# Optimization experiments

Measured on AMD Instinct MI355X. Metric: run time of the kernel, lower is better.

## Reference

```python
import jax, jax.numpy as jnp
import numpy as np

NUM_OBJ_CLS = 9  # len(anchor_scales) * len(anchor_ratios) = 3 * 3


def _bce_with_logits_sum(x, y):
    # Numerically stable BCEWithLogitsLoss(reduction='sum'):
    # max(x,0) - x*y + log(1 + exp(-|x|)), summed over all elements.
    return jnp.sum(jnp.maximum(x, 0.0) - x * y + jnp.log1p(jnp.exp(-jnp.abs(x))))


def setup_inputs() -> dict:
    key = jax.random.key(0)
    k1, k2, k3 = jax.random.split(key, 3)
    B, H, W = 16, 192, 192
    pred = jax.random.normal(k1, (B, 6 * NUM_OBJ_CLS, H, W), dtype=jnp.float32)
    target = jax.random.uniform(k2, (B, 6, H, W), dtype=jnp.float32)
    loc = jax.random.randint(k3, (128, 2), 0, H)  # (x, y) coords into HxW map
    return {"pred": pred, "target": target, "loc": loc}


def reference(pred, target, loc):
    # Objectness loss: for i in range(0, 18, 2):
    #   BCE_sum(pred[:, i], target[:, 0]) + BCE_sum(pred[:, i+1], target[:, 1])
    # then divided by NUM_OBJ_CLS. Even channels pair with target ch 0,
    # odd channels with target ch 1. Vectorized over the 9 anchor classes.
    even = pred[:, 0:2 * NUM_OBJ_CLS:2]   # [B, 9, H, W]
    odd = pred[:, 1:2 * NUM_OBJ_CLS:2]    # [B, 9, H, W]
    t0 = target[:, 0:1]                    # [B, 1, H, W] broadcasts over 9
    t1 = target[:, 1:2]
    loss_obj = (_bce_with_logits_sum(even, t0) + _bce_with_logits_sum(odd, t1))
    loss_obj = loss_obj / NUM_OBJ_CLS
    # NOTE: in the original module the box-loss branch computes pred_box /
    # target_box gathers inside python loops but never accumulates them into
    # loss_box, which stays 0. Faithfully, the output is loss_obj alone; loc
    # does not affect the result.
    return loss_obj
```

## Files before the change

kernel.cpp:

```cpp
#include <hip/hip_runtime.h>
#include <hip/hip_bf16.h>


#define HW_     (192 * 192)
#define HW4_    (HW_ / 4)
#define NCH_    18
#define PREDC_  54
#define TGTC_   6
#define NB_     16

__device__ __forceinline__ float bce_elem(float x, float y) {
    return fmaxf(x, 0.0f) - x * y + log1pf(__expf(-fabsf(x)));
}

__global__ __launch_bounds__(256) void rpn_bce_kernel(
        const float* __restrict__ pred,
        const float* __restrict__ target,
        float* __restrict__ out) {
    const int total = NB_ * NCH_ * HW4_;
    const int stride = gridDim.x * blockDim.x;

    const float4* __restrict__ p4 = (const float4*)pred;
    const float4* __restrict__ t4 = (const float4*)target;

    float acc = 0.0f;
    for (int i = blockIdx.x * blockDim.x + threadIdx.x; i < total; i += stride) {
        int b  = i / (NCH_ * HW4_);
        int r  = i - b * (NCH_ * HW4_);
        int c  = r / HW4_;
        int hw = r - c * HW4_;

        float4 x = p4[(b * PREDC_ + c) * HW4_ + hw];
        float4 y = t4[(b * TGTC_ + (c & 1)) * HW4_ + hw];

        acc += bce_elem(x.x, y.x);
        acc += bce_elem(x.y, y.y);
        acc += bce_elem(x.z, y.z);
        acc += bce_elem(x.w, y.w);
    }

    #pragma unroll
    for (int off = 32; off > 0; off >>= 1)
        acc += __shfl_down(acc, off, 64);

    __shared__ float wsum[4];
    const int lane = threadIdx.x & 63;
    const int wid  = threadIdx.x >> 6;
    if (lane == 0) wsum[wid] = acc;
    __syncthreads();

    if (threadIdx.x == 0) {
        float s = wsum[0] + wsum[1] + wsum[2] + wsum[3];
        atomicAdd(out, s * (1.0f / 9.0f));
    }
}

extern "C" void kernel_launch(void* const* d_in, const int* in_sizes, int n_in,
                              void* d_out, int out_size, void* d_ws, size_t ws_size,
                              hipStream_t stream) {
    const float* pred   = (const float*)d_in[0];
    const float* target = (const float*)d_in[1];
    float* out = (float*)d_out;

    hipMemsetAsync(out, 0, sizeof(float), stream);

    rpn_bce_kernel<<<2048, 256, 0, stream>>>(pred, target, out);
}
```

Before: 188.6 us.

## Reuse target load across nine anchor channels and drop grid-stride loop

Each thread now owns one (parity, batch, position) float4 of the target. It loads that target value once and loops, unrolled, over the nine anchor channels of matching parity. This replaces the grid-stride loop and its per-iteration integer divisions, removes redundant target reads, and exposes nine independent loads per thread. The launch grows to one thread per target vector (1152 blocks), with one atomic per block. log1pf is also swapped for the cheaper __logf(1+t), which is slightly less accurate.

```diff
diff --git a/kernel.cpp b/kernel.cpp
--- a/kernel.cpp
+++ b/kernel.cpp
@@ -1,38 +1,41 @@
 #include <hip/hip_runtime.h>
-#include <hip/hip_bf16.h>
 
 
-#define HW_     (192 * 192)
-#define HW4_    (HW_ / 4)
-#define NCH_    18
+#define HW4_    9216
+#define NB_     16
 #define PREDC_  54
 #define TGTC_   6
-#define NB_     16
+#define NPAIR_  9
+#define POS_    (NB_ * HW4_)
+#define NTHREADS_ (2 * POS_)
+#define NBLOCKS_  (NTHREADS_ / 256)
 
 __device__ __forceinline__ float bce_elem(float x, float y) {
-    return fmaxf(x, 0.0f) - x * y + log1pf(__expf(-fabsf(x)));
+    float t = __expf(-fabsf(x));
+    return fmaxf(x, 0.0f) - x * y + __logf(1.0f + t);
 }
 
 __global__ __launch_bounds__(256) void rpn_bce_kernel(
         const float* __restrict__ pred,
         const float* __restrict__ target,
         float* __restrict__ out) {
-    const int total = NB_ * NCH_ * HW4_;
-    const int stride = gridDim.x * blockDim.x;
+    const int tid = blockIdx.x * 256 + threadIdx.x;
+    const int par = tid / POS_;
+    const int pos = tid - par * POS_;
+    const int b   = pos / HW4_;
+    const int hw  = pos - b * HW4_;
 
     const float4* __restrict__ p4 = (const float4*)pred;
     const float4* __restrict__ t4 = (const float4*)target;
 
+    const float4 y = t4[(b * TGTC_ + par) * HW4_ + hw];
+
+    const float4* px = p4 + (b * PREDC_ + par) * HW4_ + hw;
+
     float acc = 0.0f;
-    for (int i = blockIdx.x * blockDim.x + threadIdx.x; i < total; i += stride) {
-        int b  = i / (NCH_ * HW4_);
-        int r  = i - b * (NCH_ * HW4_);
-        int c  = r / HW4_;
-        int hw = r - c * HW4_;
-
-        float4 x = p4[(b * PREDC_ + c) * HW4_ + hw];
-        float4 y = t4[(b * TGTC_ + (c & 1)) * HW4_ + hw];
-
+    #pragma unroll
+    for (int k = 0; k < NPAIR_; ++k) {
+        float4 x = px[2 * k * HW4_];
         acc += bce_elem(x.x, y.x);
         acc += bce_elem(x.y, y.y);
         acc += bce_elem(x.z, y.z);
@@ -64,5 +67,5 @@
 
     hipMemsetAsync(out, 0, sizeof(float), stream);
 
-    rpn_bce_kernel<<<2048, 256, 0, stream>>>(pred, target, out);
+    rpn_bce_kernel<<<NBLOCKS_, 256, 0, stream>>>(pred, target, out);
 }
```

Result: faster. 182.5 us (-3.2%).
